# Kernel tuning notes

Hardware: AMD Instinct MI355X
Metric: run time of the kernel (lower is better)

The kernel has to match this reference:

```python
import jax, jax.numpy as jnp
import numpy as np

CR = 4; D = 768; H = 12; DH = 64; L = 3; I = 3072
W1S = 128  # one-sided sliding window = config.attention_window(256) // 2 (transformers convention)
MAXPOS = 7200; MLP = 512; NCLS = 3
EPS = 1e-12

def layer_norm(x, s, b):
    m = jnp.mean(x, -1, keepdims=True)
    v = jnp.var(x, -1, keepdims=True)
    return (x - m) * jax.lax.rsqrt(v + EPS) * s + b

def band_attention(q, k, v, w):
    # q,k,v: [B,H,S,dh]; each token attends to +-w neighbors (Longformer sliding chunks, no global tokens)
    B, Hh, S, dh = q.shape
    nc = S // w
    qc = q.reshape(B, Hh, nc, w, dh)
    kp = jnp.pad(k, ((0, 0), (0, 0), (w, w), (0, 0)))
    vp = jnp.pad(v, ((0, 0), (0, 0), (w, w), (0, 0)))
    idx = jnp.arange(nc)[:, None] * w + jnp.arange(3 * w)[None, :]          # [nc, 3w]
    kc = kp[:, :, idx]                                                      # [B,H,nc,3w,dh]
    vc = vp[:, :, idx]
    scores = jnp.einsum('bhcqd,bhckd->bhcqk', qc, kc) / np.float32(np.sqrt(dh))
    rel = jnp.arange(3 * w)[None, :] - w - jnp.arange(w)[:, None]           # [w,3w] key_pos - query_pos
    kpos = jnp.arange(nc)[:, None, None] * w + jnp.arange(3 * w)[None, None, :] - w
    mask = (jnp.abs(rel)[None] <= w) & (kpos >= 0) & (kpos < S)             # [nc,w,3w]
    scores = jnp.where(mask[None, None], scores, jnp.float32(-1e9))
    probs = jax.nn.softmax(scores, axis=-1)
    out = jnp.einsum('bhcqk,bhckd->bhcqd', probs, vc)
    return out.reshape(B, Hh, S, dh)

def forward(x, proj_w, proj_b, pos_emb, tok_emb, emb_ln_s, emb_ln_b,
            wq, bq, wk, bk, wv, bv, wo, bo, ln1_s, ln1_b,
            wi, bi, wo2, bo2, ln2_s, ln2_b,
            pool_w, pool_b, head_ln_s, head_ln_b, head_w1, head_b1, head_w2, head_b2):
    n, c, t, wd, hh = x.shape
    tc, sc = t // CR, wd // CR
    # torch unfold(dim, size, step) with size==step == contiguous block reshape
    xr = x[:, :, :tc * CR].reshape(n, c, CR, tc, CR, sc, CR, sc)
    xr = xr.transpose(0, 1, 2, 4, 6, 3, 5, 7)            # n,c,cr_t,cr_w,cr_h,tc,sc,sc
    xr = xr.reshape(n, c, CR ** 3, tc * sc * sc)
    xr = xr.transpose(0, 3, 2, 1).reshape(n, tc * sc * sc, CR ** 3 * c)
    h = xr @ proj_w + proj_b                             # [B,S,D]
    B, S = h.shape[0], h.shape[1]
    pos_ids = jnp.arange(S) % (MAXPOS - 2)               # no padding: S is already a multiple of 2w
    h = h + pos_emb[pos_ids][None] + tok_emb[0][None, None]
    h = layer_norm(h, emb_ln_s, emb_ln_b)
    for l in range(L):
        q = (h @ wq[l] + bq[l]).reshape(B, S, H, DH).transpose(0, 2, 1, 3)
        k = (h @ wk[l] + bk[l]).reshape(B, S, H, DH).transpose(0, 2, 1, 3)
        v = (h @ wv[l] + bv[l]).reshape(B, S, H, DH).transpose(0, 2, 1, 3)
        a = band_attention(q, k, v, W1S).transpose(0, 2, 1, 3).reshape(B, S, D)
        h = layer_norm(h + a @ wo[l] + bo[l], ln1_s[l], ln1_b[l])
        f = jax.nn.gelu(h @ wi[l] + bi[l], approximate=False) @ wo2[l] + bo2[l]
        h = layer_norm(h + f, ln2_s[l], ln2_b[l])
    pooled = jnp.tanh(h[:, 0] @ pool_w + pool_b)         # LongformerPooler on first token
    z = layer_norm(pooled, head_ln_s, head_ln_b)
    z = jax.nn.gelu(z @ head_w1 + head_b1, approximate=False)
    return z @ head_w2 + head_b2                         # [B, num_classes]

def setup_inputs() -> dict:
    key = jax.random.key(0)
    ks = iter(jax.random.split(key, 40))
    p = lambda *s: jax.random.normal(next(ks), s, jnp.float32) * 0.02
    d = {
        'x': jax.random.normal(next(ks), (8, 3, 64, 32, 32), jnp.float32),
        'position_ids': jnp.tile(jnp.arange(1024, dtype=jnp.int32)[None], (8, 1)),
        'proj_w': p(3 * CR ** 3, D), 'proj_b': p(D),
        'pos_emb': p(MAXPOS, D), 'tok_emb': p(2, D),
        'emb_ln_s': jnp.ones((D,), jnp.float32), 'emb_ln_b': jnp.zeros((D,), jnp.float32),
        'wq': p(L, D, D), 'bq': p(L, D), 'wk': p(L, D, D), 'bk': p(L, D),
        'wv': p(L, D, D), 'bv': p(L, D), 'wo': p(L, D, D), 'bo': p(L, D),
        'ln1_s': jnp.ones((L, D), jnp.float32), 'ln1_b': jnp.zeros((L, D), jnp.float32),
        'wi': p(L, D, I), 'bi': p(L, I), 'wo2': p(L, I, D), 'bo2': p(L, D),
        'ln2_s': jnp.ones((L, D), jnp.float32), 'ln2_b': jnp.zeros((L, D), jnp.float32),
        'pool_w': p(D, D), 'pool_b': p(D),
        'head_ln_s': jnp.ones((D,), jnp.float32), 'head_ln_b': jnp.zeros((D,), jnp.float32),
        'head_w1': p(D, MLP), 'head_b1': p(MLP),
        'head_w2': p(MLP, NCLS), 'head_b2': p(NCLS),
    }
    return d

def reference(x, position_ids, proj_w, proj_b, pos_emb, tok_emb, emb_ln_s, emb_ln_b,
              wq, bq, wk, bk, wv, bv, wo, bo, ln1_s, ln1_b,
              wi, bi, wo2, bo2, ln2_s, ln2_b,
              pool_w, pool_b, head_ln_s, head_ln_b, head_w1, head_b1, head_w2, head_b2):
    # position_ids is overwritten inside the spat_temp branch of the original forward (arange over cuboids)
    return forward(x, proj_w, proj_b, pos_emb, tok_emb, emb_ln_s, emb_ln_b,
                   wq, bq, wk, bk, wv, bv, wo, bo, ln1_s, ln1_b,
                   wi, bi, wo2, bo2, ln2_s, ln2_b,
                   pool_w, pool_b, head_ln_s, head_ln_b, head_w1, head_b1, head_w2, head_b2)
```

## Files before the change

### kernel.cpp

```cpp
#include <hip/hip_runtime.h>
#include <hip/hip_bf16.h>
#include <math.h>


typedef __attribute__((ext_vector_type(8))) short short8;
typedef __attribute__((ext_vector_type(4))) short short4v;
typedef __attribute__((ext_vector_type(4))) float floatx4;

__device__ __forceinline__ float gelu_exact(float x) {
    return 0.5f * x * (1.f + erff(x * 0.70710678118654752440f));
}

__device__ __forceinline__ short bfs(float x) {
    __hip_bfloat16 h = __float2bfloat16(x);
    short s;
    __builtin_memcpy(&s, &h, 2);
    return s;
}

__device__ __forceinline__ float bf2f(short s) {
    unsigned u = ((unsigned)(unsigned short)s) << 16;
    float f;
    __builtin_memcpy(&f, &u, 4);
    return f;
}

#define GLOAD_LDS16(g, l) __builtin_amdgcn_global_load_lds( \
    (const __attribute__((address_space(1))) void*)(g),     \
    (__attribute__((address_space(3))) void*)(l), 16, 0, 0)

__global__ __launch_bounds__(256) void transpose_bf16(
    const float* __restrict__ W, __hip_bfloat16* __restrict__ Wt,
    int K, int N, long inLS, long outLS)
{
    __shared__ float tile[32][33];
    int l = blockIdx.z;
    const float* Wl = W + (long)l * inLS;
    __hip_bfloat16* Wtl = Wt + (long)l * outLS;
    int lx = threadIdx.x & 31, ly = threadIdx.x >> 5;
    int kb = blockIdx.y * 32, nb = blockIdx.x * 32;
    #pragma unroll
    for (int r = 0; r < 32; r += 8)
        tile[ly + r][lx] = Wl[(long)(kb + ly + r) * N + nb + lx];
    __syncthreads();
    #pragma unroll
    for (int r = 0; r < 32; r += 8)
        Wtl[(long)(nb + ly + r) * K + kb + lx] = __float2bfloat16(tile[lx][ly + r]);
}

__global__ void pack_qkv_bias(const float* __restrict__ bq,
                              const float* __restrict__ bk,
                              const float* __restrict__ bv,
                              float* __restrict__ out)
{
    int l = blockIdx.x, tid = threadIdx.x;
    out[l * 2304 + tid]        = bq[l * 768 + tid];
    out[l * 2304 + 768 + tid]  = bk[l * 768 + tid];
    out[l * 2304 + 1536 + tid] = bv[l * 768 + tid];
}

__global__ __launch_bounds__(192) void gather_x(
    const float* __restrict__ x, __hip_bfloat16* __restrict__ xr)
{
    int tok = blockIdx.x;
    int b = tok >> 10, s = tok & 1023;
    int tci = s >> 6, sci = (s >> 3) & 7, scj = s & 7;
    int f = threadIdx.x;
    int ch  = f % 3;
    int crc = f / 3;
    int cr1 = crc >> 4, cr2 = (crc >> 2) & 3, cr3 = crc & 3;
    float v = x[(((b * 3 + ch) * 64) + cr1 * 16 + tci) * 1024 +
                (cr2 * 8 + sci) * 32 + cr3 * 8 + scj];
    xr[(long)tok * 192 + f] = __float2bfloat16(v);
}

template<int ACT, typename OT>
__global__ __launch_bounds__(256) void mfma_gemm(
    const __hip_bfloat16* __restrict__ A, const __hip_bfloat16* __restrict__ Bt,
    const float* __restrict__ bias, OT* __restrict__ C, int M, int N, int K)
{
    __shared__ __hip_bfloat16 As[128 * 32];
    __shared__ __hip_bfloat16 Bs[128 * 32];
    int tid  = threadIdx.x;
    int wave = tid >> 6, lane = tid & 63;
    long m0 = (long)blockIdx.y * 128, n0 = (long)blockIdx.x * 128;
    int wr = wave >> 1, wc = wave & 1;
    floatx4 acc[4][4] = {};

    int srow = (wave * 128 + lane) >> 2;
    int sch  = lane & 3;
    const __hip_bfloat16* Ag = A  + (m0 + srow) * K + sch * 8;
    const __hip_bfloat16* Bg = Bt + (n0 + srow) * K + sch * 8;
    __hip_bfloat16* AsW = &As[wave * 128 * 8];
    __hip_bfloat16* BsW = &Bs[wave * 128 * 8];
    int lm = lane & 15, lk8 = (lane >> 4) * 8;

    for (int k0 = 0; k0 < K; k0 += 32) {
        GLOAD_LDS16(Ag + k0,          AsW);
        GLOAD_LDS16(Ag + 16 * K + k0, AsW + 64 * 8);
        GLOAD_LDS16(Bg + k0,          BsW);
        GLOAD_LDS16(Bg + 16 * K + k0, BsW + 64 * 8);
        __syncthreads();
        short8 af[4], bf[4];
        #pragma unroll
        for (int mi = 0; mi < 4; mi++)
            af[mi] = *(const short8*)&As[(wr * 64 + mi * 16 + lm) * 32 + lk8];
        #pragma unroll
        for (int ni = 0; ni < 4; ni++)
            bf[ni] = *(const short8*)&Bs[(wc * 64 + ni * 16 + lm) * 32 + lk8];
        #pragma unroll
        for (int mi = 0; mi < 4; mi++)
            #pragma unroll
            for (int ni = 0; ni < 4; ni++)
                acc[mi][ni] = __builtin_amdgcn_mfma_f32_16x16x32_bf16(
                    af[mi], bf[ni], acc[mi][ni], 0, 0, 0);
        __syncthreads();
    }

    int colb = (int)n0 + wc * 64 + lm;
    int rowb = (int)m0 + wr * 64 + (lane >> 4) * 4;
    #pragma unroll
    for (int ni = 0; ni < 4; ni++) {
        int col = colb + ni * 16;
        float bv = bias[col];
        #pragma unroll
        for (int mi = 0; mi < 4; mi++) {
            #pragma unroll
            for (int j = 0; j < 4; j++) {
                float o = acc[mi][ni][j] + bv;
                if (ACT == 1) o = gelu_exact(o);
                long idx = (long)(rowb + mi * 16 + j) * N + col;
                if constexpr (sizeof(OT) == 2) C[idx] = __float2bfloat16(o);
                else                           C[idx] = o;
            }
        }
    }
}

__global__ __launch_bounds__(256) void pos_ln_kernel(
    const float* __restrict__ t, const float* __restrict__ pos_emb,
    const float* __restrict__ tok_emb, const float* __restrict__ ln_s,
    const float* __restrict__ ln_b, float* __restrict__ h,
    __hip_bfloat16* __restrict__ hbf)
{
    int tok = blockIdx.x;
    int s = tok & 1023;
    int tid = threadIdx.x;
    __shared__ float red[8];
    const float* trow = &t[(long)tok * 768];
    int d0 = tid, d1 = tid + 256, d2 = tid + 512;
    float a0 = trow[d0] + pos_emb[s * 768 + d0] + tok_emb[d0];
    float a1 = trow[d1] + pos_emb[s * 768 + d1] + tok_emb[d1];
    float a2 = trow[d2] + pos_emb[s * 768 + d2] + tok_emb[d2];
    float sum = a0 + a1 + a2;
    float sumsq = a0 * a0 + a1 * a1 + a2 * a2;
    #pragma unroll
    for (int off = 32; off; off >>= 1) {
        sum   += __shfl_down(sum, off, 64);
        sumsq += __shfl_down(sumsq, off, 64);
    }
    if ((tid & 63) == 0) { red[tid >> 6] = sum; red[4 + (tid >> 6)] = sumsq; }
    __syncthreads();
    sum   = red[0] + red[1] + red[2] + red[3];
    sumsq = red[4] + red[5] + red[6] + red[7];
    float mean = sum * (1.f / 768.f);
    float var  = sumsq * (1.f / 768.f) - mean * mean;
    float rs   = rsqrtf(var + 1e-12f);
    float* hrow = &h[(long)tok * 768];
    __hip_bfloat16* brow = &hbf[(long)tok * 768];
    float o0 = (a0 - mean) * rs * ln_s[d0] + ln_b[d0];
    float o1 = (a1 - mean) * rs * ln_s[d1] + ln_b[d1];
    float o2 = (a2 - mean) * rs * ln_s[d2] + ln_b[d2];
    hrow[d0] = o0; hrow[d1] = o1; hrow[d2] = o2;
    brow[d0] = __float2bfloat16(o0);
    brow[d1] = __float2bfloat16(o1);
    brow[d2] = __float2bfloat16(o2);
}

__global__ __launch_bounds__(256) void attn_kernel(
    const __hip_bfloat16* __restrict__ QKV, __hip_bfloat16* __restrict__ Ob)
{
    __shared__ __hip_bfloat16 KV[128 * 72];
    __shared__ __hip_bfloat16 Pl[4][32 * 136];
    __shared__ float alpha_s[4][32];
    __shared__ float l_s[4][32];

    int blk = blockIdx.x;
    int ci = blk & 7, hh = (blk >> 3) % 12, b = blk / 96;
    int tid = threadIdx.x, w = tid >> 6, lane = tid & 63;
    int lm = lane & 15, lg = lane >> 4;
    __hip_bfloat16* Pw = &Pl[w][0];

    short8 qf[2][2];
    #pragma unroll
    for (int nt = 0; nt < 2; nt++) {
        int q = ci * 128 + w * 32 + nt * 16 + lm;
        const __hip_bfloat16* qp = &QKV[((long)(b * 1024 + q)) * 2304 + hh * 64];
        #pragma unroll
        for (int ks = 0; ks < 2; ks++)
            qf[nt][ks] = *(const short8*)(qp + ks * 32 + lg * 8);
    }

    floatx4 accO[2][4] = {};
    float m_run[2] = {-1e30f, -1e30f};
    float l_run[2] = {0.f, 0.f};

    for (int tt = 0; tt < 3; tt++) {
        __syncthreads();
        #pragma unroll
        for (int i = 0; i < 4; i++) {
            int e = tid + i * 256;
            int jj = e >> 3, dd = (e & 7) * 8;
            int kpos = ci * 128 + tt * 128 + jj - 128;
            short8 kv = {};
            if (kpos >= 0 && kpos < 1024)
                kv = *(const short8*)&QKV[((long)(b * 1024 + kpos)) * 2304 + 768 + hh * 64 + dd];
            *(short8*)&KV[jj * 72 + dd] = kv;
        }
        __syncthreads();

        floatx4 accS[8][2] = {};
        #pragma unroll
        for (int ks = 0; ks < 2; ks++)
            #pragma unroll
            for (int mt = 0; mt < 8; mt++) {
                short8 kf = *(const short8*)&KV[(mt * 16 + lm) * 72 + ks * 32 + lg * 8];
                accS[mt][0] = __builtin_amdgcn_mfma_f32_16x16x32_bf16(kf, qf[0][ks], accS[mt][0], 0, 0, 0);
                accS[mt][1] = __builtin_amdgcn_mfma_f32_16x16x32_bf16(kf, qf[1][ks], accS[mt][1], 0, 0, 0);
            }

        float tmax[2] = {-1e30f, -1e30f};
        #pragma unroll
        for (int nt = 0; nt < 2; nt++) {
            int r = w * 32 + nt * 16 + lm;
            #pragma unroll
            for (int mt = 0; mt < 8; mt++)
                #pragma unroll
                for (int j = 0; j < 4; j++) {
                    int jrel = tt * 128 + mt * 16 + lg * 4 + j;
                    int kpos = ci * 128 + jrel - 128;
                    bool valid = (jrel >= r) && (jrel <= r + 256) &&
                                 (kpos >= 0) && (kpos < 1024);
                    float s = valid ? accS[mt][nt][j] * 0.125f : -1e9f;
                    accS[mt][nt][j] = s;
                    tmax[nt] = fmaxf(tmax[nt], s);
                }
            tmax[nt] = fmaxf(tmax[nt], __shfl_xor(tmax[nt], 16));
            tmax[nt] = fmaxf(tmax[nt], __shfl_xor(tmax[nt], 32));
        }

        float al[2];
        #pragma unroll
        for (int nt = 0; nt < 2; nt++) {
            float mnew = fmaxf(m_run[nt], tmax[nt]);
            al[nt] = __expf(m_run[nt] - mnew);
            m_run[nt] = mnew;
            float ts = 0.f;
            #pragma unroll
            for (int mt = 0; mt < 8; mt++) {
                short4v pp;
                #pragma unroll
                for (int j = 0; j < 4; j++) {
                    float p = __expf(accS[mt][nt][j] - mnew);
                    ts += p;
                    pp[j] = bfs(p);
                }
                *(short4v*)&Pw[(nt * 16 + lm) * 136 + mt * 16 + lg * 4] = pp;
            }
            ts += __shfl_xor(ts, 16);
            ts += __shfl_xor(ts, 32);
            l_run[nt] = l_run[nt] * al[nt] + ts;
        }
        if (lg < 2) alpha_s[w][lg * 16 + lm] = al[lg];

        __syncthreads();
        #pragma unroll
        for (int i = 0; i < 4; i++) {
            int e = tid + i * 256;
            int jj = e >> 3, dd = (e & 7) * 8;
            int kpos = ci * 128 + tt * 128 + jj - 128;
            short8 vv = {};
            if (kpos >= 0 && kpos < 1024)
                vv = *(const short8*)&QKV[((long)(b * 1024 + kpos)) * 2304 + 1536 + hh * 64 + dd];
            short* kvs = (short*)KV;
            #pragma unroll
            for (int m2 = 0; m2 < 8; m2++)
                kvs[(dd + m2) * 136 + jj] = vv[m2];
        }
        __syncthreads();

        #pragma unroll
        for (int mo = 0; mo < 2; mo++)
            #pragma unroll
            for (int j = 0; j < 4; j++) {
                float a = alpha_s[w][mo * 16 + lg * 4 + j];
                #pragma unroll
                for (int nd = 0; nd < 4; nd++)
                    accO[mo][nd][j] *= a;
            }

        #pragma unroll
        for (int kk = 0; kk < 4; kk++) {
            short8 pf[2], vf[4];
            #pragma unroll
            for (int mo = 0; mo < 2; mo++)
                pf[mo] = *(const short8*)&Pw[(mo * 16 + lm) * 136 + kk * 32 + lg * 8];
            #pragma unroll
            for (int nd = 0; nd < 4; nd++)
                vf[nd] = *(const short8*)&KV[(nd * 16 + lm) * 136 + kk * 32 + lg * 8];
            #pragma unroll
            for (int mo = 0; mo < 2; mo++)
                #pragma unroll
                for (int nd = 0; nd < 4; nd++)
                    accO[mo][nd] = __builtin_amdgcn_mfma_f32_16x16x32_bf16(
                        pf[mo], vf[nd], accO[mo][nd], 0, 0, 0);
        }
    }

    if (lg < 2) l_s[w][lg * 16 + lm] = l_run[lg];
    #pragma unroll
    for (int mo = 0; mo < 2; mo++)
        #pragma unroll
        for (int j = 0; j < 4; j++) {
            int qr = mo * 16 + lg * 4 + j;
            float rl = 1.f / l_s[w][qr];
            int q  = w * 32 + qr;
            long base = ((long)(b * 1024 + ci * 128 + q)) * 768 + hh * 64;
            #pragma unroll
            for (int nd = 0; nd < 4; nd++)
                Ob[base + nd * 16 + lm] = __float2bfloat16(accO[mo][nd][j] * rl);
        }
}

__global__ __launch_bounds__(256) void add_ln_kernel(
    float* __restrict__ h, const float* __restrict__ t,
    const float* __restrict__ ln_s, const float* __restrict__ ln_b,
    __hip_bfloat16* __restrict__ hbf)
{
    int tok = blockIdx.x;
    int tid = threadIdx.x;
    __shared__ float red[8];
    float* hrow = &h[(long)tok * 768];
    const float* trow = &t[(long)tok * 768];
    int d0 = tid, d1 = tid + 256, d2 = tid + 512;
    float a0 = hrow[d0] + trow[d0];
    float a1 = hrow[d1] + trow[d1];
    float a2 = hrow[d2] + trow[d2];
    float sum = a0 + a1 + a2;
    float sumsq = a0 * a0 + a1 * a1 + a2 * a2;
    #pragma unroll
    for (int off = 32; off; off >>= 1) {
        sum   += __shfl_down(sum, off, 64);
        sumsq += __shfl_down(sumsq, off, 64);
    }
    if ((tid & 63) == 0) { red[tid >> 6] = sum; red[4 + (tid >> 6)] = sumsq; }
    __syncthreads();
    sum   = red[0] + red[1] + red[2] + red[3];
    sumsq = red[4] + red[5] + red[6] + red[7];
    float mean = sum * (1.f / 768.f);
    float var  = sumsq * (1.f / 768.f) - mean * mean;
    float rs   = rsqrtf(var + 1e-12f);
    __hip_bfloat16* brow = &hbf[(long)tok * 768];
    float o0 = (a0 - mean) * rs * ln_s[d0] + ln_b[d0];
    float o1 = (a1 - mean) * rs * ln_s[d1] + ln_b[d1];
    float o2 = (a2 - mean) * rs * ln_s[d2] + ln_b[d2];
    hrow[d0] = o0; hrow[d1] = o1; hrow[d2] = o2;
    brow[d0] = __float2bfloat16(o0);
    brow[d1] = __float2bfloat16(o1);
    brow[d2] = __float2bfloat16(o2);
}

__global__ __launch_bounds__(256) void pool_split(
    const __hip_bfloat16* __restrict__ hbf, const __hip_bfloat16* __restrict__ pool_wt,
    const float* __restrict__ pool_b, float* __restrict__ pooled)
{
    int g = blockIdx.x * 256 + threadIdx.x;
    int out = g >> 3, t8 = g & 7;
    int b = out / 768, d = out - b * 768;
    const __hip_bfloat16* hr = hbf + (long)b * 1024 * 768;
    const __hip_bfloat16* wr = pool_wt + (long)d * 768;
    float acc = 0.f;
    #pragma unroll
    for (int kk = 0; kk < 96; kk += 8) {
        int k = t8 * 96 + kk;
        short8 hv = *(const short8*)&hr[k];
        short8 wv = *(const short8*)&wr[k];
        #pragma unroll
        for (int j = 0; j < 8; j++) acc += bf2f(hv[j]) * bf2f(wv[j]);
    }
    acc += __shfl_down(acc, 4, 64);
    acc += __shfl_down(acc, 2, 64);
    acc += __shfl_down(acc, 1, 64);
    if (t8 == 0) pooled[out] = tanhf(acc + pool_b[d]);
}

__global__ __launch_bounds__(256) void ln_z_kernel(
    const float* __restrict__ pooled, const float* __restrict__ hln_s,
    const float* __restrict__ hln_b, __hip_bfloat16* __restrict__ zbf)
{
    int b = blockIdx.x, tid = threadIdx.x;
    __shared__ float red[8];
    const float* pr = &pooled[b * 768];
    float p0 = pr[tid], p1 = pr[tid + 256], p2 = pr[tid + 512];
    float sum = p0 + p1 + p2;
    float sumsq = p0 * p0 + p1 * p1 + p2 * p2;
    #pragma unroll
    for (int off = 32; off; off >>= 1) {
        sum   += __shfl_down(sum, off, 64);
        sumsq += __shfl_down(sumsq, off, 64);
    }
    if ((tid & 63) == 0) { red[tid >> 6] = sum; red[4 + (tid >> 6)] = sumsq; }
    __syncthreads();
    sum   = red[0] + red[1] + red[2] + red[3];
    sumsq = red[4] + red[5] + red[6] + red[7];
    float mean = sum * (1.f / 768.f);
    float var  = sumsq * (1.f / 768.f) - mean * mean;
    float rs   = rsqrtf(var + 1e-12f);
    zbf[b * 768 + tid]       = __float2bfloat16((p0 - mean) * rs * hln_s[tid]       + hln_b[tid]);
    zbf[b * 768 + tid + 256] = __float2bfloat16((p1 - mean) * rs * hln_s[tid + 256] + hln_b[tid + 256]);
    zbf[b * 768 + tid + 512] = __float2bfloat16((p2 - mean) * rs * hln_s[tid + 512] + hln_b[tid + 512]);
}

__global__ __launch_bounds__(256) void mlp_split(
    const __hip_bfloat16* __restrict__ zbf, const __hip_bfloat16* __restrict__ w1t,
    const float* __restrict__ b1, float* __restrict__ z1)
{
    int g = blockIdx.x * 256 + threadIdx.x;
    int out = g >> 3, t8 = g & 7;
    int b = out >> 9, d = out & 511;
    const __hip_bfloat16* zr = zbf + b * 768;
    const __hip_bfloat16* wr = w1t + (long)d * 768;
    float acc = 0.f;
    #pragma unroll
    for (int kk = 0; kk < 96; kk += 8) {
        int k = t8 * 96 + kk;
        short8 zv = *(const short8*)&zr[k];
        short8 wv = *(const short8*)&wr[k];
        #pragma unroll
        for (int j = 0; j < 8; j++) acc += bf2f(zv[j]) * bf2f(wv[j]);
    }
    acc += __shfl_down(acc, 4, 64);
    acc += __shfl_down(acc, 2, 64);
    acc += __shfl_down(acc, 1, 64);
    if (t8 == 0) z1[out] = gelu_exact(acc + b1[d]);
}

__global__ __launch_bounds__(256) void head_final_kernel(
    const float* __restrict__ z1, const float* __restrict__ w2,
    const float* __restrict__ b2, float* __restrict__ out)
{
    int tid = threadIdx.x;
    int g = tid >> 3, t8 = tid & 7;
    if (g < 24) {
        int b = g / 3, o = g % 3;
        float acc = 0.f;
        for (int k = t8; k < 512; k += 8)
            acc += z1[b * 512 + k] * w2[k * 3 + o];
        acc += __shfl_down(acc, 4, 64);
        acc += __shfl_down(acc, 2, 64);
        acc += __shfl_down(acc, 1, 64);
        if (t8 == 0) out[b * 3 + o] = acc + b2[o];
    }
}

extern "C" void kernel_launch(void* const* d_in, const int* in_sizes, int n_in,
                              void* d_out, int out_size, void* d_ws, size_t ws_size,
                              hipStream_t stream) {
    const float* x       = (const float*)d_in[0];
    const float* proj_w  = (const float*)d_in[2];
    const float* proj_b  = (const float*)d_in[3];
    const float* pos_emb = (const float*)d_in[4];
    const float* tok_emb = (const float*)d_in[5];
    const float* eln_s   = (const float*)d_in[6];
    const float* eln_b   = (const float*)d_in[7];
    const float* wq      = (const float*)d_in[8];
    const float* bq      = (const float*)d_in[9];
    const float* wk      = (const float*)d_in[10];
    const float* bk      = (const float*)d_in[11];
    const float* wv      = (const float*)d_in[12];
    const float* bv      = (const float*)d_in[13];
    const float* wo      = (const float*)d_in[14];
    const float* bo      = (const float*)d_in[15];
    const float* ln1_s   = (const float*)d_in[16];
    const float* ln1_b   = (const float*)d_in[17];
    const float* wi      = (const float*)d_in[18];
    const float* bi      = (const float*)d_in[19];
    const float* wo2     = (const float*)d_in[20];
    const float* bo2     = (const float*)d_in[21];
    const float* ln2_s   = (const float*)d_in[22];
    const float* ln2_b   = (const float*)d_in[23];
    const float* pool_w  = (const float*)d_in[24];
    const float* pool_b  = (const float*)d_in[25];
    const float* hln_s   = (const float*)d_in[26];
    const float* hln_b   = (const float*)d_in[27];
    const float* hw1     = (const float*)d_in[28];
    const float* hb1     = (const float*)d_in[29];
    const float* hw2     = (const float*)d_in[30];
    const float* hb2     = (const float*)d_in[31];

    char* wp = (char*)d_ws;
    auto alloc = [&](size_t bytes) {
        char* p = wp; wp += (bytes + 255) & ~(size_t)255; return p;
    };
    float*          h       = (float*)alloc(8192ll * 768 * 4);
    __hip_bfloat16* qkv_bf  = (__hip_bfloat16*)alloc(8192ll * 2304 * 2);
    float*          t       = (float*)alloc(8192ll * 768 * 4);
    __hip_bfloat16* mlp_bf  = (__hip_bfloat16*)alloc(8192ll * 3072 * 2);
    __hip_bfloat16* h_bf    = (__hip_bfloat16*)alloc(8192ll * 768 * 2);
    __hip_bfloat16* a_bf    = (__hip_bfloat16*)alloc(8192ll * 768 * 2);
    __hip_bfloat16* qkvw_t  = (__hip_bfloat16*)alloc(3ll * 2304 * 768 * 2);
    __hip_bfloat16* wo_t    = (__hip_bfloat16*)alloc(3ll * 768 * 768 * 2);
    __hip_bfloat16* wi_t    = (__hip_bfloat16*)alloc(3ll * 3072 * 768 * 2);
    __hip_bfloat16* wo2_t   = (__hip_bfloat16*)alloc(3ll * 768 * 3072 * 2);
    float*          qkv_b   = (float*)alloc(3ll * 2304 * 4);
    __hip_bfloat16* xr_bf   = (__hip_bfloat16*)alloc(8192ll * 192 * 2);
    __hip_bfloat16* projw_t = (__hip_bfloat16*)alloc(768ll * 192 * 2);
    __hip_bfloat16* poolw_t = (__hip_bfloat16*)alloc(768ll * 768 * 2);
    __hip_bfloat16* w1_t    = (__hip_bfloat16*)alloc(512ll * 768 * 2);
    float*          pooled  = (float*)alloc(8ll * 768 * 4);
    __hip_bfloat16* z_bf    = (__hip_bfloat16*)alloc(8ll * 768 * 2);
    float*          z1      = (float*)alloc(8ll * 512 * 4);

    transpose_bf16<<<dim3(24, 24, 3), 256, 0, stream>>>(wq, qkvw_t,               768, 768,  768ll * 768,  2304ll * 768);
    transpose_bf16<<<dim3(24, 24, 3), 256, 0, stream>>>(wk, qkvw_t + 768 * 768,   768, 768,  768ll * 768,  2304ll * 768);
    transpose_bf16<<<dim3(24, 24, 3), 256, 0, stream>>>(wv, qkvw_t + 1536 * 768,  768, 768,  768ll * 768,  2304ll * 768);
    transpose_bf16<<<dim3(24, 24, 3), 256, 0, stream>>>(wo, wo_t,                 768, 768,  768ll * 768,  768ll * 768);
    transpose_bf16<<<dim3(96, 24, 3), 256, 0, stream>>>(wi, wi_t,                 768, 3072, 768ll * 3072, 3072ll * 768);
    transpose_bf16<<<dim3(24, 96, 3), 256, 0, stream>>>(wo2, wo2_t,               3072, 768, 3072ll * 768, 768ll * 3072);
    transpose_bf16<<<dim3(24, 6, 1),  256, 0, stream>>>(proj_w, projw_t,          192, 768,  0, 0);
    transpose_bf16<<<dim3(24, 24, 1), 256, 0, stream>>>(pool_w, poolw_t,          768, 768,  0, 0);
    transpose_bf16<<<dim3(16, 24, 1), 256, 0, stream>>>(hw1, w1_t,                768, 512,  0, 0);
    pack_qkv_bias<<<3, 768, 0, stream>>>(bq, bk, bv, qkv_b);

    gather_x<<<8192, 192, 0, stream>>>(x, xr_bf);
    mfma_gemm<0, float><<<dim3(6, 64), 256, 0, stream>>>(
        xr_bf, projw_t, proj_b, t, 8192, 768, 192);
    pos_ln_kernel<<<8192, 256, 0, stream>>>(t, pos_emb, tok_emb, eln_s, eln_b, h, h_bf);

    for (int l = 0; l < 3; l++) {
        mfma_gemm<0, __hip_bfloat16><<<dim3(18, 64), 256, 0, stream>>>(
            h_bf, qkvw_t + (long)l * 2304 * 768, qkv_b + l * 2304, qkv_bf,
            8192, 2304, 768);
        attn_kernel<<<768, 256, 0, stream>>>(qkv_bf, a_bf);
        mfma_gemm<0, float><<<dim3(6, 64), 256, 0, stream>>>(
            a_bf, wo_t + (long)l * 768 * 768, bo + l * 768, t,
            8192, 768, 768);
        add_ln_kernel<<<8192, 256, 0, stream>>>(h, t, ln1_s + l * 768, ln1_b + l * 768, h_bf);
        mfma_gemm<1, __hip_bfloat16><<<dim3(24, 64), 256, 0, stream>>>(
            h_bf, wi_t + (long)l * 3072 * 768, bi + l * 3072, mlp_bf,
            8192, 3072, 768);
        mfma_gemm<0, float><<<dim3(6, 64), 256, 0, stream>>>(
            mlp_bf, wo2_t + (long)l * 768 * 3072, bo2 + l * 768, t,
            8192, 768, 3072);
        add_ln_kernel<<<8192, 256, 0, stream>>>(h, t, ln2_s + l * 768, ln2_b + l * 768, h_bf);
    }

    pool_split<<<192, 256, 0, stream>>>(h_bf, poolw_t, pool_b, pooled);
    ln_z_kernel<<<8, 256, 0, stream>>>(pooled, hln_s, hln_b, z_bf);
    mlp_split<<<128, 256, 0, stream>>>(z_bf, w1_t, hb1, z1);
    head_final_kernel<<<1, 256, 0, stream>>>(z1, hw2, hb2, (float*)d_out);
}
```

Before: 1.225 ms.

## Swizzle GEMM LDS, stage epilogue through LDS, emit bf16 outputs, remap blocks

The GEMM now XOR-swizzles the LDS layout to cut bank conflicts on fragment reads. Its epilogue stages results through padded LDS so rows are written to global memory as coalesced 16-byte bf16 vectors. All intermediate projection outputs (t) become bf16 instead of fp32, halving that traffic for the residual/LayerNorm kernels. Blocks use a 1D grid with M-major ordering so neighbouring blocks share B tiles. The trade-off is some extra precision loss in the residual branch and extra syncs in the epilogue.

```diff
diff --git a/kernel.cpp b/kernel.cpp
--- a/kernel.cpp
+++ b/kernel.cpp
@@ -74,26 +74,30 @@
     xr[(long)tok * 192 + f] = __float2bfloat16(v);
 }
 
-template<int ACT, typename OT>
+template<int ACT>
 __global__ __launch_bounds__(256) void mfma_gemm(
     const __hip_bfloat16* __restrict__ A, const __hip_bfloat16* __restrict__ Bt,
-    const float* __restrict__ bias, OT* __restrict__ C, int M, int N, int K)
-{
-    __shared__ __hip_bfloat16 As[128 * 32];
-    __shared__ __hip_bfloat16 Bs[128 * 32];
+    const float* __restrict__ bias, __hip_bfloat16* __restrict__ C,
+    int M, int N, int K)
+{
+    __shared__ short lds_raw[8704];
+    __hip_bfloat16* As = (__hip_bfloat16*)lds_raw;
+    __hip_bfloat16* Bs = As + 4096;
     int tid  = threadIdx.x;
     int wave = tid >> 6, lane = tid & 63;
-    long m0 = (long)blockIdx.y * 128, n0 = (long)blockIdx.x * 128;
+    int L = blockIdx.x;
+    long m0 = (long)(L & 63) * 128, n0 = (long)(L >> 6) * 128;
     int wr = wave >> 1, wc = wave & 1;
     floatx4 acc[4][4] = {};
 
     int srow = (wave * 128 + lane) >> 2;
-    int sch  = lane & 3;
+    int sch  = (lane & 3) ^ ((lane >> 3) & 3);
     const __hip_bfloat16* Ag = A  + (m0 + srow) * K + sch * 8;
     const __hip_bfloat16* Bg = Bt + (n0 + srow) * K + sch * 8;
     __hip_bfloat16* AsW = &As[wave * 128 * 8];
     __hip_bfloat16* BsW = &Bs[wave * 128 * 8];
-    int lm = lane & 15, lk8 = (lane >> 4) * 8;
+    int lm = lane & 15, lg = lane >> 4;
+    int lk8 = ((lg ^ ((lm >> 1) & 3))) * 8;
 
     for (int k0 = 0; k0 < K; k0 += 32) {
         GLOAD_LDS16(Ag + k0,          AsW);
@@ -117,28 +121,40 @@
         __syncthreads();
     }
 
-    int colb = (int)n0 + wc * 64 + lm;
-    int rowb = (int)m0 + wr * 64 + (lane >> 4) * 4;
-    #pragma unroll
-    for (int ni = 0; ni < 4; ni++) {
-        int col = colb + ni * 16;
-        float bv = bias[col];
-        #pragma unroll
-        for (int mi = 0; mi < 4; mi++) {
-            #pragma unroll
-            for (int j = 0; j < 4; j++) {
-                float o = acc[mi][ni][j] + bv;
-                if (ACT == 1) o = gelu_exact(o);
-                long idx = (long)(rowb + mi * 16 + j) * N + col;
-                if constexpr (sizeof(OT) == 2) C[idx] = __float2bfloat16(o);
-                else                           C[idx] = o;
-            }
-        }
+    float bvv[4];
+    #pragma unroll
+    for (int ni = 0; ni < 4; ni++)
+        bvv[ni] = bias[n0 + wc * 64 + ni * 16 + lm];
+    int erow = tid >> 4;
+    int ecol = (tid & 15) * 8;
+    #pragma unroll
+    for (int p = 0; p < 2; p++) {
+        if (wr == p) {
+            #pragma unroll
+            for (int mi = 0; mi < 4; mi++)
+                #pragma unroll
+                for (int ni = 0; ni < 4; ni++)
+                    #pragma unroll
+                    for (int j = 0; j < 4; j++) {
+                        float o = acc[mi][ni][j] + bvv[ni];
+                        if (ACT == 1) o = gelu_exact(o);
+                        lds_raw[(mi * 16 + lg * 4 + j) * 136 +
+                                wc * 64 + ni * 16 + lm] = bfs(o);
+                    }
+        }
+        __syncthreads();
+        #pragma unroll
+        for (int rr = 0; rr < 4; rr++) {
+            int r = erow + rr * 16;
+            short8 v = *(const short8*)&lds_raw[r * 136 + ecol];
+            *(short8*)&C[(m0 + p * 64 + r) * N + n0 + ecol] = v;
+        }
+        __syncthreads();
     }
 }
 
 __global__ __launch_bounds__(256) void pos_ln_kernel(
-    const float* __restrict__ t, const float* __restrict__ pos_emb,
+    const __hip_bfloat16* __restrict__ t, const float* __restrict__ pos_emb,
     const float* __restrict__ tok_emb, const float* __restrict__ ln_s,
     const float* __restrict__ ln_b, float* __restrict__ h,
     __hip_bfloat16* __restrict__ hbf)
@@ -147,11 +163,11 @@
     int s = tok & 1023;
     int tid = threadIdx.x;
     __shared__ float red[8];
-    const float* trow = &t[(long)tok * 768];
+    const __hip_bfloat16* trow = &t[(long)tok * 768];
     int d0 = tid, d1 = tid + 256, d2 = tid + 512;
-    float a0 = trow[d0] + pos_emb[s * 768 + d0] + tok_emb[d0];
-    float a1 = trow[d1] + pos_emb[s * 768 + d1] + tok_emb[d1];
-    float a2 = trow[d2] + pos_emb[s * 768 + d2] + tok_emb[d2];
+    float a0 = __bfloat162float(trow[d0]) + pos_emb[s * 768 + d0] + tok_emb[d0];
+    float a1 = __bfloat162float(trow[d1]) + pos_emb[s * 768 + d1] + tok_emb[d1];
+    float a2 = __bfloat162float(trow[d2]) + pos_emb[s * 768 + d2] + tok_emb[d2];
     float sum = a0 + a1 + a2;
     float sumsq = a0 * a0 + a1 * a1 + a2 * a2;
     #pragma unroll
@@ -333,7 +349,7 @@
 }
 
 __global__ __launch_bounds__(256) void add_ln_kernel(
-    float* __restrict__ h, const float* __restrict__ t,
+    float* __restrict__ h, const __hip_bfloat16* __restrict__ t,
     const float* __restrict__ ln_s, const float* __restrict__ ln_b,
     __hip_bfloat16* __restrict__ hbf)
 {
@@ -341,11 +357,11 @@
     int tid = threadIdx.x;
     __shared__ float red[8];
     float* hrow = &h[(long)tok * 768];
-    const float* trow = &t[(long)tok * 768];
+    const __hip_bfloat16* trow = &t[(long)tok * 768];
     int d0 = tid, d1 = tid + 256, d2 = tid + 512;
-    float a0 = hrow[d0] + trow[d0];
-    float a1 = hrow[d1] + trow[d1];
-    float a2 = hrow[d2] + trow[d2];
+    float a0 = hrow[d0] + __bfloat162float(trow[d0]);
+    float a1 = hrow[d1] + __bfloat162float(trow[d1]);
+    float a2 = hrow[d2] + __bfloat162float(trow[d2]);
     float sum = a0 + a1 + a2;
     float sumsq = a0 * a0 + a1 * a1 + a2 * a2;
     #pragma unroll
@@ -504,7 +520,7 @@
     };
     float*          h       = (float*)alloc(8192ll * 768 * 4);
     __hip_bfloat16* qkv_bf  = (__hip_bfloat16*)alloc(8192ll * 2304 * 2);
-    float*          t       = (float*)alloc(8192ll * 768 * 4);
+    __hip_bfloat16* t_bf    = (__hip_bfloat16*)alloc(8192ll * 768 * 2);
     __hip_bfloat16* mlp_bf  = (__hip_bfloat16*)alloc(8192ll * 3072 * 2);
     __hip_bfloat16* h_bf    = (__hip_bfloat16*)alloc(8192ll * 768 * 2);
     __hip_bfloat16* a_bf    = (__hip_bfloat16*)alloc(8192ll * 768 * 2);
@@ -533,26 +549,26 @@
     pack_qkv_bias<<<3, 768, 0, stream>>>(bq, bk, bv, qkv_b);
 
     gather_x<<<8192, 192, 0, stream>>>(x, xr_bf);
-    mfma_gemm<0, float><<<dim3(6, 64), 256, 0, stream>>>(
-        xr_bf, projw_t, proj_b, t, 8192, 768, 192);
-    pos_ln_kernel<<<8192, 256, 0, stream>>>(t, pos_emb, tok_emb, eln_s, eln_b, h, h_bf);
+    mfma_gemm<0><<<6 * 64, 256, 0, stream>>>(
+        xr_bf, projw_t, proj_b, t_bf, 8192, 768, 192);
+    pos_ln_kernel<<<8192, 256, 0, stream>>>(t_bf, pos_emb, tok_emb, eln_s, eln_b, h, h_bf);
 
     for (int l = 0; l < 3; l++) {
-        mfma_gemm<0, __hip_bfloat16><<<dim3(18, 64), 256, 0, stream>>>(
+        mfma_gemm<0><<<18 * 64, 256, 0, stream>>>(
             h_bf, qkvw_t + (long)l * 2304 * 768, qkv_b + l * 2304, qkv_bf,
             8192, 2304, 768);
         attn_kernel<<<768, 256, 0, stream>>>(qkv_bf, a_bf);
-        mfma_gemm<0, float><<<dim3(6, 64), 256, 0, stream>>>(
-            a_bf, wo_t + (long)l * 768 * 768, bo + l * 768, t,
+        mfma_gemm<0><<<6 * 64, 256, 0, stream>>>(
+            a_bf, wo_t + (long)l * 768 * 768, bo + l * 768, t_bf,
             8192, 768, 768);
-        add_ln_kernel<<<8192, 256, 0, stream>>>(h, t, ln1_s + l * 768, ln1_b + l * 768, h_bf);
-        mfma_gemm<1, __hip_bfloat16><<<dim3(24, 64), 256, 0, stream>>>(
+        add_ln_kernel<<<8192, 256, 0, stream>>>(h, t_bf, ln1_s + l * 768, ln1_b + l * 768, h_bf);
+        mfma_gemm<1><<<24 * 64, 256, 0, stream>>>(
             h_bf, wi_t + (long)l * 3072 * 768, bi + l * 3072, mlp_bf,
             8192, 3072, 768);
-        mfma_gemm<0, float><<<dim3(6, 64), 256, 0, stream>>>(
-            mlp_bf, wo2_t + (long)l * 768 * 3072, bo2 + l * 768, t,
+        mfma_gemm<0><<<6 * 64, 256, 0, stream>>>(
+            mlp_bf, wo2_t + (long)l * 768 * 3072, bo2 + l * 768, t_bf,
             8192, 768, 3072);
-        add_ln_kernel<<<8192, 256, 0, stream>>>(h, t, ln2_s + l * 768, ln2_b + l * 768, h_bf);
+        add_ln_kernel<<<8192, 256, 0, stream>>>(h, t_bf, ln2_s + l * 768, ln2_b + l * 768, h_bf);
     }
 
     pool_split<<<192, 256, 0, stream>>>(h_bf, poolw_t, pool_b, pooled);
```

After: 1.195 ms. -2.4%, faster.
